# Kernel optimization log

Measured on AMD Instinct MI355X. Metric: run time of the kernel, lower is better.

## Reference

```python
import jax, jax.numpy as jnp
import numpy as np

FP8_MAX = 448.0  # float8_e4m3fn max normal
BLOCK = 128

def quant_dequant(x, block_size=BLOCK):
    """Block-wise fp8 (e4m3) activation/kernel quantization along last dim,
    immediately dequantized (mathematically equivalent to fp8 GEMM with
    per-block scales applied during accumulation)."""
    *lead, d = x.shape
    xb = x.reshape(*lead, d // block_size, block_size)
    scale = jnp.max(jnp.abs(xb), axis=-1, keepdims=True) / FP8_MAX
    scale = jnp.maximum(scale, 1e-12)
    q = (xb / scale).astype(jnp.float8_e4m3fn).astype(x.dtype)
    return (q * scale).reshape(x.shape)

def fp8_linear(x, W, b, block_size=BLOCK):
    y = jnp.dot(quant_dequant(x, block_size), quant_dequant(W, block_size))
    return y + b

def setup_inputs() -> dict:
    key = jax.random.key(0)
    ks = jax.random.split(key, 3)
    B, S, D = 2, 2048, 1024
    x = jax.random.normal(ks[0], (B, S, D), dtype=jnp.float32)
    W_qkv = jax.random.normal(ks[1], (D, 3 * D), dtype=jnp.float32) * (1.0 / np.sqrt(D))
    b_qkv = jnp.zeros((3 * D,), dtype=jnp.float32)
    W_out = jax.random.normal(ks[2], (D, D), dtype=jnp.float32) * (1.0 / np.sqrt(D))
    b_out = jnp.zeros((D,), dtype=jnp.float32)
    return {"x": x, "W_qkv": W_qkv, "b_qkv": b_qkv, "W_out": W_out, "b_out": b_out}

def reference(x, W_qkv, b_qkv, W_out, b_out):
    NUM_HEADS, HEAD_DIM = 16, 64
    B, S, _ = x.shape
    # fp8-quantized QKV projection
    qkv = fp8_linear(x, W_qkv, b_qkv)                       # [B,S,3*H*Dh]
    qkv = qkv.reshape(B, S, 3, NUM_HEADS, HEAD_DIM).transpose(2, 0, 3, 1, 4)
    q, k, v = qkv[0], qkv[1], qkv[2]                        # each [B,H,S,Dh]
    scale = 1.0 / jnp.sqrt(jnp.float32(HEAD_DIM)).astype(x.dtype)
    attn = jnp.einsum('bhqd,bhkd->bhqk', q, k) * scale      # [B,H,S,S]
    attn = jax.nn.softmax(attn, axis=-1)
    out = jnp.einsum('bhqk,bhkd->bhqd', attn, v)            # [B,H,S,Dh]
    out = out.transpose(0, 2, 1, 3).reshape(B, S, NUM_HEADS * HEAD_DIM)
    # fp8-quantized output projection; present (kv cache) is None here
    return fp8_linear(out, W_out, b_out)
```

## Files before the change

### kernel.cpp

```cpp
#include <hip/hip_runtime.h>
#include <cstdint>
#include <cstddef>

typedef __attribute__((ext_vector_type(8))) short bfrag;
typedef __attribute__((ext_vector_type(8))) _Float16 hfrag;
typedef __attribute__((ext_vector_type(2))) __fp16 fp16x2;
typedef __attribute__((ext_vector_type(4))) float f4;
typedef __attribute__((ext_vector_type(16))) float f16v;
typedef __attribute__((ext_vector_type(4))) unsigned short us4;

#define MFMA16H(a, b, c) __builtin_amdgcn_mfma_f32_16x16x32_f16(a, b, c, 0, 0, 0)
#define MFMA32H(a, b, c) __builtin_amdgcn_mfma_f32_32x32x16_f16(a, b, c, 0, 0, 0)

__device__ __forceinline__ unsigned cvt_pkrtz_u(float a, float b) {
  union { fp16x2 h; unsigned u; } c;
  c.h = __builtin_amdgcn_cvt_pkrtz(a, b);
  return c.u;
}
__device__ __forceinline__ unsigned short f2h_bits(float x) {
  _Float16 h = (_Float16)x;
  union { _Float16 h; unsigned short u; } c;
  c.h = h;
  return c.u;
}
__device__ __forceinline__ float h2f(unsigned short u) {
  union { unsigned short u; _Float16 h; } c;
  c.u = u;
  return (float)c.h;
}
__device__ __forceinline__ void permswap(unsigned& a, unsigned& b) {
  auto r = __builtin_amdgcn_permlane32_swap((int)a, (int)b, false, false);
  a = (unsigned)r[0];
  b = (unsigned)r[1];
}
__device__ __forceinline__ void gl16(const unsigned short* g, unsigned short* l) {
  __builtin_amdgcn_global_load_lds(
      (const __attribute__((address_space(1))) unsigned int*)g,
      (__attribute__((address_space(3))) unsigned int*)l, 16, 0, 0);
}
__device__ __forceinline__ float max3f(float a, float b, float c) {
  float r;
  asm("v_max3_f32 %0, %1, %2, %3" : "=v"(r) : "v"(a), "v"(b), "v"(c));
  return r;
}
__device__ __forceinline__ float exp2_fast(float x) {
  float r;
  asm("v_exp_f32 %0, %1" : "=v"(r) : "v"(x));
  return r;
}

__device__ __forceinline__ float qd_e4m3(float v) {
  float a = fabsf(v);
  unsigned u = __float_as_uint(a);
  int e = (int)(u >> 23) - 127;
  int k = e - 3;
  if (k < -9) k = -9;
  float big = __uint_as_float((unsigned)(k + 150) << 23);
  float r = (a + big) - big;
  return __builtin_copysignf(r, v);
}

__global__ __launch_bounds__(256) void quant_x(const float* __restrict__ src,
                                               unsigned short* __restrict__ q,
                                               float* __restrict__ s,
                                               int nblk) {
  int gid = blockIdx.x * 256 + threadIdx.x;
  int wid = gid >> 6;
  int lane = gid & 63;
  if (wid >= nblk) return;
  size_t off = (size_t)wid * 128 + lane * 2;
  float2 xv = *reinterpret_cast<const float2*>(src + off);
  float m = fmaxf(fabsf(xv.x), fabsf(xv.y));
#pragma unroll
  for (int d = 32; d > 0; d >>= 1) m = fmaxf(m, __shfl_xor(m, d));
  float scale = fmaxf(m / 448.0f, 1e-12f);
  unsigned short q0 = f2h_bits(qd_e4m3(xv.x / scale));
  unsigned short q1 = f2h_bits(qd_e4m3(xv.y / scale));
  *reinterpret_cast<unsigned*>(q + off) = (unsigned)q0 | ((unsigned)q1 << 16);
  if (lane == 0) s[wid] = scale;
}

__global__ __launch_bounds__(256) void quant_xh(const unsigned short* __restrict__ src,
                                                unsigned short* __restrict__ q,
                                                float* __restrict__ s,
                                                int nblk) {
  int gid = blockIdx.x * 256 + threadIdx.x;
  int wid = gid >> 6;
  int lane = gid & 63;
  if (wid >= nblk) return;
  size_t off = (size_t)wid * 128 + lane * 2;
  unsigned hv = *reinterpret_cast<const unsigned*>(src + off);
  float x0 = h2f((unsigned short)(hv & 0xffffu));
  float x1 = h2f((unsigned short)(hv >> 16));
  float m = fmaxf(fabsf(x0), fabsf(x1));
#pragma unroll
  for (int d = 32; d > 0; d >>= 1) m = fmaxf(m, __shfl_xor(m, d));
  float scale = fmaxf(m / 448.0f, 1e-12f);
  unsigned short q0 = f2h_bits(qd_e4m3(x0 / scale));
  unsigned short q1 = f2h_bits(qd_e4m3(x1 / scale));
  *reinterpret_cast<unsigned*>(q + off) = (unsigned)q0 | ((unsigned)q1 << 16);
  if (lane == 0) s[wid] = scale;
}

__global__ __launch_bounds__(256) void quant_w_t(const float* __restrict__ W,
                                                 unsigned short* __restrict__ WT,
                                                 int K, int N) {
  __shared__ __align__(16) unsigned short Ht[128][72];
  const int tid = threadIdx.x;
  const int w = tid >> 6, l = tid & 63;
  const int k0 = blockIdx.y * 64, n0 = blockIdx.x * 128;
#pragma unroll 4
  for (int i = 0; i < 16; ++i) {
    int kl = w * 16 + i;
    float2 xv = *reinterpret_cast<const float2*>(&W[(size_t)(k0 + kl) * N + n0 + l * 2]);
    float m = fmaxf(fabsf(xv.x), fabsf(xv.y));
#pragma unroll
    for (int d = 32; d > 0; d >>= 1) m = fmaxf(m, __shfl_xor(m, d));
    float scale = fmaxf(m / 448.0f, 1e-12f);
    Ht[l * 2][kl]     = f2h_bits(qd_e4m3(xv.x / scale) * scale);
    Ht[l * 2 + 1][kl] = f2h_bits(qd_e4m3(xv.y / scale) * scale);
  }
  __syncthreads();
  const int n = tid & 127, hs = tid >> 7;
  unsigned short* dst = WT + (size_t)(n0 + n) * K + k0 + hs * 32;
#pragma unroll
  for (int j = 0; j < 4; ++j)
    *reinterpret_cast<bfrag*>(dst + j * 8) =
        *reinterpret_cast<const bfrag*>(&Ht[n][hs * 32 + j * 8]);
}

template <int MF, bool SPLIT>
__global__ __launch_bounds__(256, 2) void gemm_q(const unsigned short* __restrict__ Aq,
                                                 const float* __restrict__ As,
                                                 const unsigned short* __restrict__ WT,
                                                 const float* __restrict__ bias,
                                                 float* __restrict__ Cf,
                                                 unsigned short* __restrict__ C16,
                                                 int M, int N, int K) {
  constexpr int MT = MF * 32;
  __shared__ __align__(16) unsigned short Al[MT][64];
  __shared__ __align__(16) unsigned short Bh[128][64];
  __shared__ float Ss[MT][8];
  const int tid = threadIdx.x;
  const int w = tid >> 6, l = tid & 63;
  const int lr = l & 15, lg = l >> 4;
  const int nbx = N >> 7;
  const int nwg = nbx * (M / MT);
  const int q8 = nwg >> 3;
  const int swz = ((int)blockIdx.x & 7) * q8 + ((int)blockIdx.x >> 3);
  const int row0 = (swz / nbx) * MT, col0 = (swz % nbx) << 7;
  const int wr = (w >> 1) * (MT / 2), wc = (w & 1) * 64;
  const int xsw = (lr & 7) * 8;

  if (MF == 4) {
    int r = tid >> 1, c0 = (tid & 1) * 4;
    *reinterpret_cast<float4*>(&Ss[r][c0]) =
        *reinterpret_cast<const float4*>(&As[(size_t)(row0 + r) * 8 + c0]);
  } else {
    int r = tid >> 2, c0 = (tid & 3) * 2;
    *reinterpret_cast<float2*>(&Ss[r][c0]) =
        *reinterpret_cast<const float2*>(&As[(size_t)(row0 + r) * 8 + c0]);
  }

  f4 acc[MF][4], seg[MF][4];
#pragma unroll
  for (int i = 0; i < MF; ++i)
#pragma unroll
    for (int j = 0; j < 4; ++j)
#pragma unroll
      for (int c = 0; c < 4; ++c) {
        acc[i][j][c] = 0.f;
        seg[i][j][c] = 0.f;
      }

  const int lrow = l >> 3;
  const int jch = (l & 7) ^ lrow;
  const unsigned short* pA = Aq + (size_t)(row0 + w * (MT / 4) + lrow) * K + jch * 8;
  const unsigned short* pH = WT + (size_t)(col0 + w * 32 + lrow) * K + jch * 8;
  unsigned short* dA = &Al[0][0] + w * (MT / 4) * 64;
  unsigned short* dH = &Bh[0][0] + w * 2048;

  const int niter = K >> 6;
  for (int it = 0; it < niter; ++it) {
    const int k0 = it << 6;
    __syncthreads();
#pragma unroll
    for (int ii = 0; ii < MF; ++ii)
      gl16(pA + (size_t)ii * 8 * K + k0, dA + ii * 512);
#pragma unroll
    for (int ii = 0; ii < 4; ++ii)
      gl16(pH + (size_t)ii * 8 * K + k0, dH + ii * 512);
    __syncthreads();

#pragma unroll
    for (int ks = 0; ks < 2; ++ks) {
      hfrag af[MF];
#pragma unroll
      for (int mf = 0; mf < MF; ++mf)
        af[mf] = *reinterpret_cast<const hfrag*>(
            &Al[0][0] + (wr + mf * 16 + lr) * 64 + ((ks * 32 + lg * 8) ^ xsw));
#pragma unroll
      for (int nf = 0; nf < 4; ++nf) {
        hfrag bh = *reinterpret_cast<const hfrag*>(
            &Bh[0][0] + (wc + nf * 16 + lr) * 64 + ((ks * 32 + lg * 8) ^ xsw));
#pragma unroll
        for (int mf = 0; mf < MF; ++mf)
          seg[mf][nf] = MFMA16H(af[mf], bh, seg[mf][nf]);
      }
    }

    if (it & 1) {
      const int kb = it >> 1;
#pragma unroll
      for (int mf = 0; mf < MF; ++mf) {
        float sv[4];
#pragma unroll
        for (int r = 0; r < 4; ++r) sv[r] = Ss[wr + mf * 16 + lg * 4 + r][kb];
#pragma unroll
        for (int nf = 0; nf < 4; ++nf)
#pragma unroll
          for (int r = 0; r < 4; ++r) {
            acc[mf][nf][r] += sv[r] * seg[mf][nf][r];
            seg[mf][nf][r] = 0.f;
          }
      }
    }
  }

#pragma unroll
  for (int mf = 0; mf < MF; ++mf) {
#pragma unroll
    for (int r = 0; r < 4; ++r) {
      const int m = row0 + wr + mf * 16 + lg * 4 + r;
#pragma unroll
      for (int nf = 0; nf < 4; ++nf) {
        const int col = col0 + wc + nf * 16 + lr;
        float o = acc[mf][nf][r] + bias[col];
        if (SPLIT) {
          C16[(size_t)m * N + col] = f2h_bits(o);
        } else {
          Cf[(size_t)m * N + col] = o;
        }
      }
    }
  }
}

__global__ __launch_bounds__(256, 2) void attn_mfma32(const unsigned short* __restrict__ qkv,
                                                      unsigned short* __restrict__ out16) {
  __shared__ __align__(16) unsigned short Vth[2][64][40];
  const int tid = threadIdx.x;
  const int w = tid >> 6, l = tid & 63;
  const int q = l & 31;
  const int hi = l >> 5;
  const int lin = (int)blockIdx.x;
  const int xcd = lin & 7, j = lin >> 3;
  const int bh = 4 * xcd + (j >> 4);
  const int qt = j & 15;
  const int q0 = qt * 128 + w * 32;
  const int b = bh >> 4, h = bh & 15;
  const size_t bbase = (size_t)b * 2048;
  const size_t hoff = (size_t)h * 64;
  const float C = 0.18033688011112042f;

  const int rA = (q & 24) | ((q + (q >> 3)) & 7);
  const int rB = 32 + ((q & 24) | ((q + 4 + (q >> 3)) & 7));

  hfrag qh[4];
  {
    const size_t qrow = (bbase + q0 + q) * 3072 + hoff + hi * 8;
#pragma unroll
    for (int f = 0; f < 4; ++f)
      qh[f] = *reinterpret_cast<const hfrag*>(qkv + qrow + f * 16);
  }

  const int skp = tid >> 3;
  const int sc = tid & 7;

  const unsigned short* kph = qkv + (bbase + q) * 3072 + 1024 + hoff + hi * 8;
  const unsigned short* vph = qkv + (bbase + skp) * 3072 + 2048 + hoff + sc * 8;
  const size_t KSTEP = (size_t)32 * 3072;

  hfrag kh[4];
  bfrag svh;

#pragma unroll
  for (int f = 0; f < 4; ++f)
    kh[f] = *reinterpret_cast<const hfrag*>(kph + f * 16);
  svh = *reinterpret_cast<const bfrag*>(vph);
  vph += KSTEP;
#pragma unroll
  for (int j2 = 0; j2 < 8; ++j2) {
    int row = sc * 8 + ((j2 + sc) & 7);
    Vth[0][row][skp] = (unsigned short)svh[j2];
  }
  f16v sA, sB;
#pragma unroll
  for (int r = 0; r < 16; ++r) sA[r] = 0.f;
  __builtin_amdgcn_s_setprio(1);
#pragma unroll
  for (int f = 0; f < 4; ++f) sA = MFMA32H(kh[f], qh[f], sA);
  __builtin_amdgcn_s_setprio(0);
  kph += KSTEP;
#pragma unroll
  for (int f = 0; f < 4; ++f)
    kh[f] = *reinterpret_cast<const hfrag*>(kph + f * 16);
  __syncthreads();

  f16v oA0, oA1;
#pragma unroll
  for (int r = 0; r < 16; ++r) { oA0[r] = 0.f; oA1[r] = 0.f; }
  float m2 = -1e30f, l_i = 0.f;

#define ATTN_ITER(KT, SCUR, SNXT)                                              \
  do {                                                                         \
    const int kt_ = (KT);                                                      \
    const int cur_ = kt_ & 1;                                                  \
         \
    if (kt_ < 63) {                                                            \
      _Pragma("unroll") for (int r = 0; r < 16; ++r) SNXT[r] = 0.f;            \
      __builtin_amdgcn_s_setprio(1);                                           \
      _Pragma("unroll") for (int f = 0; f < 4; ++f)                            \
          SNXT = MFMA32H(kh[f], qh[f], SNXT);                                  \
      __builtin_amdgcn_s_setprio(0);                                           \
    }                                                                          \
                                                         \
    if (kt_ < 62) {                                                            \
      kph += KSTEP;                                                            \
      _Pragma("unroll") for (int f = 0; f < 4; ++f)                            \
          kh[f] = *reinterpret_cast<const hfrag*>(kph + f * 16);               \
    }                                                                          \
                             \
    float t0 = max3f(SCUR[0], SCUR[1], SCUR[2]);                               \
    float t1 = max3f(SCUR[3], SCUR[4], SCUR[5]);                               \
    float t2 = max3f(SCUR[6], SCUR[7], SCUR[8]);                               \
    float t3 = max3f(SCUR[9], SCUR[10], SCUR[11]);                             \
    float t4 = max3f(SCUR[12], SCUR[13], SCUR[14]);                            \
    float u0 = max3f(t0, t1, SCUR[15]);                                        \
    float u1 = max3f(t2, t3, t4);                                              \
    float mt = fmaxf(u0, u1);                                                  \
    mt = fmaxf(mt, __shfl_xor(mt, 32));                                        \
    float mt2 = mt * C;                                                        \
    if (!__all(mt2 <= m2)) {           \
      float mn = fmaxf(m2, mt2);                                               \
      float corr = exp2_fast(m2 - mn);                                         \
      m2 = mn;                                                                 \
      l_i *= corr;                                                             \
      _Pragma("unroll") for (int r = 0; r < 16; ++r) {                         \
        oA0[r] *= corr; oA1[r] *= corr;                                        \
      }                                                                        \
    }                                                                          \
    float p[16];                                                               \
    _Pragma("unroll") for (int r = 0; r < 16; ++r)                             \
        p[r] = exp2_fast(fmaf(SCUR[r], C, -m2));                               \
    float r0_ = (p[0] + p[1]) + (p[2] + p[3]);                                 \
    float r1_ = (p[4] + p[5]) + (p[6] + p[7]);                                 \
    float r2_ = (p[8] + p[9]) + (p[10] + p[11]);                               \
    float r3_ = (p[12] + p[13]) + (p[14] + p[15]);                             \
    float rs = (r0_ + r1_) + (r2_ + r3_);                                      \
    rs += __shfl_xor(rs, 32);                                                  \
    l_i += rs;                                                                 \
                         \
    if (kt_ < 63) {                                                            \
      svh = *reinterpret_cast<const bfrag*>(vph);                              \
      vph += KSTEP;                                                            \
    }                                                                          \
                       \
    unsigned ph_[8];                                                           \
    _Pragma("unroll") for (int i = 0; i < 8; ++i)                              \
        ph_[i] = cvt_pkrtz_u(p[2 * i], p[2 * i + 1]);                          \
    permswap(ph_[0], ph_[2]); permswap(ph_[1], ph_[3]);                        \
    permswap(ph_[4], ph_[6]); permswap(ph_[5], ph_[7]);                        \
    union U4 { unsigned u[4]; hfrag f; };                                      \
    U4 f0h, f1h;                                                               \
    f0h.u[0] = ph_[0]; f0h.u[1] = ph_[1]; f0h.u[2] = ph_[2]; f0h.u[3] = ph_[3];\
    f1h.u[0] = ph_[4]; f1h.u[1] = ph_[5]; f1h.u[2] = ph_[6]; f1h.u[3] = ph_[7];\
                         \
    __builtin_amdgcn_s_setprio(1);                                             \
    _Pragma("unroll") for (int c = 0; c < 2; ++c) {                            \
      hfrag pF = c ? f1h.f : f0h.f;                                            \
      hfrag vh0 = *reinterpret_cast<const hfrag*>(&Vth[cur_][rA][c * 16 + hi * 8]); \
      hfrag vh1 = *reinterpret_cast<const hfrag*>(&Vth[cur_][rB][c * 16 + hi * 8]); \
      oA0 = MFMA32H(vh0, pF, oA0);                                             \
      oA1 = MFMA32H(vh1, pF, oA1);                                             \
    }                                                                          \
    __builtin_amdgcn_s_setprio(0);                                             \
              \
    if (kt_ < 63) {                                                            \
      _Pragma("unroll") for (int j2 = 0; j2 < 8; ++j2) {                       \
        int row = sc * 8 + ((j2 + sc) & 7);                                    \
        Vth[cur_ ^ 1][row][skp] = (unsigned short)svh[j2];                     \
      }                                                                        \
      __syncthreads();                                                         \
    }                                                                          \
  } while (0)

  for (int kt = 0; kt < 64; kt += 2) {
    ATTN_ITER(kt, sA, sB);
    ATTN_ITER(kt + 1, sB, sA);
  }
#undef ATTN_ITER

  float inv = 1.0f / l_i;
  const size_t orow = (bbase + q0 + q) * 1024 + hoff;
#pragma unroll
  for (int dblk = 0; dblk < 2; ++dblk) {
#pragma unroll
    for (int rg = 0; rg < 4; ++rg) {
      us4 o;
#pragma unroll
      for (int e = 0; e < 4; ++e) {
        float v = (dblk == 0 ? oA0[rg * 4 + e] : oA1[rg * 4 + e]) * inv;
        o[e] = f2h_bits(v);
      }
      *reinterpret_cast<us4*>(out16 + orow + dblk * 32 + rg * 8 + hi * 4) = o;
    }
  }
}

extern "C" void kernel_launch(void* const* d_in, const int* in_sizes, int n_in,
                              void* d_out, int out_size, void* d_ws, size_t ws_size,
                              hipStream_t stream) {
  const float* x     = (const float*)d_in[0];
  const float* W_qkv = (const float*)d_in[1];
  const float* b_qkv = (const float*)d_in[2];
  const float* W_out = (const float*)d_in[3];
  const float* b_out = (const float*)d_in[4];
  float* y = (float*)d_out;

  char* ws = (char*)d_ws;
  const size_t MB = 1u << 20;
  unsigned short* x_q   = (unsigned short*)(ws);
  float*          s_x   = (float*)(ws + 8 * MB);
  unsigned short* wqh   = (unsigned short*)(ws + 8 * MB + 256 * 1024);
  unsigned short* woh   = (unsigned short*)(ws + 20 * MB + 256 * 1024);
  unsigned short* qkv   = (unsigned short*)(ws + 24 * MB + 256 * 1024);
  unsigned short* y16   = (unsigned short*)(ws + 48 * MB + 256 * 1024);

  quant_x<<<8192, 256, 0, stream>>>(x, x_q, s_x, 32768);
  quant_w_t<<<dim3(24, 16), 256, 0, stream>>>(W_qkv, wqh, 1024, 3072);
  quant_w_t<<<dim3(8, 16), 256, 0, stream>>>(W_out, woh, 1024, 1024);

  gemm_q<4, true><<<768, 256, 0, stream>>>(x_q, s_x, wqh, b_qkv,
                                           nullptr, qkv, 4096, 3072, 1024);

  attn_mfma32<<<512, 256, 0, stream>>>(qkv, y16);

  quant_xh<<<8192, 256, 0, stream>>>(y16, x_q, s_x, 32768);

  gemm_q<2, false><<<512, 256, 0, stream>>>(x_q, s_x, woh, b_out,
                                            y, nullptr, 4096, 1024, 1024);
}
```

Before: 169.0 us.

## Double attention key tile to 64 keys per iteration

Processes 64 keys per iteration instead of 32. It computes two 32-key score blocks, does one shared max/rescale step, and stages two V sub-tiles into a widened shared buffer. This halves the number of __syncthreads, online-softmax correction checks and shuffle reductions across the key loop. In exchange it raises register pressure from the doubled K fragments, scores and probabilities, which at 2 blocks per SIMD-bound launch could cause spills or lower occupancy. The LDS padding changes from 40 to 68 columns, which may alter bank conflicts.

```diff
diff --git a/kernel.cpp b/kernel.cpp
--- a/kernel.cpp
+++ b/kernel.cpp
@@ -248,7 +248,7 @@
 
 __global__ __launch_bounds__(256, 2) void attn_mfma32(const unsigned short* __restrict__ qkv,
                                                       unsigned short* __restrict__ out16) {
-  __shared__ __align__(16) unsigned short Vth[2][64][40];
+  __shared__ __align__(16) unsigned short Vth[2][64][68];
   const int tid = threadIdx.x;
   const int w = tid >> 6, l = tid & 63;
   const int q = l & 31;
@@ -277,34 +277,48 @@
   const int skp = tid >> 3;
   const int sc = tid & 7;
 
+  const size_t SUB = (size_t)32 * 3072;
+  const size_t KSTEP = (size_t)64 * 3072;
   const unsigned short* kph = qkv + (bbase + q) * 3072 + 1024 + hoff + hi * 8;
   const unsigned short* vph = qkv + (bbase + skp) * 3072 + 2048 + hoff + sc * 8;
-  const size_t KSTEP = (size_t)32 * 3072;
-
-  hfrag kh[4];
-  bfrag svh;
-
-#pragma unroll
-  for (int f = 0; f < 4; ++f)
-    kh[f] = *reinterpret_cast<const hfrag*>(kph + f * 16);
-  svh = *reinterpret_cast<const bfrag*>(vph);
+
+  hfrag kh0[4], kh1[4];
+  bfrag svh0, svh1;
+
+#define VSTAGE(BUF)                                                            \
+  do {                                                                         \
+    _Pragma("unroll") for (int j2 = 0; j2 < 8; ++j2) {                         \
+      int row = sc * 8 + ((j2 + sc) & 7);                                      \
+      Vth[BUF][row][skp] = (unsigned short)svh0[j2];                           \
+      Vth[BUF][row][32 + skp] = (unsigned short)svh1[j2];                      \
+    }                                                                          \
+  } while (0)
+
+#pragma unroll
+  for (int f = 0; f < 4; ++f) {
+    kh0[f] = *reinterpret_cast<const hfrag*>(kph + f * 16);
+    kh1[f] = *reinterpret_cast<const hfrag*>(kph + SUB + f * 16);
+  }
+  svh0 = *reinterpret_cast<const bfrag*>(vph);
+  svh1 = *reinterpret_cast<const bfrag*>(vph + SUB);
   vph += KSTEP;
-#pragma unroll
-  for (int j2 = 0; j2 < 8; ++j2) {
-    int row = sc * 8 + ((j2 + sc) & 7);
-    Vth[0][row][skp] = (unsigned short)svh[j2];
-  }
-  f16v sA, sB;
-#pragma unroll
-  for (int r = 0; r < 16; ++r) sA[r] = 0.f;
+  VSTAGE(0);
+  f16v sA0, sA1, sB0, sB1;
+#pragma unroll
+  for (int r = 0; r < 16; ++r) { sA0[r] = 0.f; sA1[r] = 0.f; }
   __builtin_amdgcn_s_setprio(1);
 #pragma unroll
-  for (int f = 0; f < 4; ++f) sA = MFMA32H(kh[f], qh[f], sA);
+  for (int f = 0; f < 4; ++f) {
+    sA0 = MFMA32H(kh0[f], qh[f], sA0);
+    sA1 = MFMA32H(kh1[f], qh[f], sA1);
+  }
   __builtin_amdgcn_s_setprio(0);
   kph += KSTEP;
 #pragma unroll
-  for (int f = 0; f < 4; ++f)
-    kh[f] = *reinterpret_cast<const hfrag*>(kph + f * 16);
+  for (int f = 0; f < 4; ++f) {
+    kh0[f] = *reinterpret_cast<const hfrag*>(kph + f * 16);
+    kh1[f] = *reinterpret_cast<const hfrag*>(kph + SUB + f * 16);
+  }
   __syncthreads();
 
   f16v oA0, oA1;
@@ -312,33 +326,44 @@
   for (int r = 0; r < 16; ++r) { oA0[r] = 0.f; oA1[r] = 0.f; }
   float m2 = -1e30f, l_i = 0.f;
 
-#define ATTN_ITER(KT, SCUR, SNXT)                                              \
+#define ATTN_ITER(KT, SC0, SC1, SN0, SN1)                                      \
   do {                                                                         \
     const int kt_ = (KT);                                                      \
     const int cur_ = kt_ & 1;                                                  \
-         \
-    if (kt_ < 63) {                                                            \
-      _Pragma("unroll") for (int r = 0; r < 16; ++r) SNXT[r] = 0.f;            \
+                  \
+    if (kt_ < 31) {                                                            \
+      _Pragma("unroll") for (int r = 0; r < 16; ++r) { SN0[r] = 0.f; SN1[r] = 0.f; } \
       __builtin_amdgcn_s_setprio(1);                                           \
-      _Pragma("unroll") for (int f = 0; f < 4; ++f)                            \
-          SNXT = MFMA32H(kh[f], qh[f], SNXT);                                  \
+      _Pragma("unroll") for (int f = 0; f < 4; ++f) {                          \
+        SN0 = MFMA32H(kh0[f], qh[f], SN0);                                     \
+        SN1 = MFMA32H(kh1[f], qh[f], SN1);                                     \
+      }                                                                        \
       __builtin_amdgcn_s_setprio(0);                                           \
     }                                                                          \
                                                          \
-    if (kt_ < 62) {                                                            \
+    if (kt_ < 30) {                                                            \
       kph += KSTEP;                                                            \
-      _Pragma("unroll") for (int f = 0; f < 4; ++f)                            \
-          kh[f] = *reinterpret_cast<const hfrag*>(kph + f * 16);               \
-    }                                                                          \
-                             \
-    float t0 = max3f(SCUR[0], SCUR[1], SCUR[2]);                               \
-    float t1 = max3f(SCUR[3], SCUR[4], SCUR[5]);                               \
-    float t2 = max3f(SCUR[6], SCUR[7], SCUR[8]);                               \
-    float t3 = max3f(SCUR[9], SCUR[10], SCUR[11]);                             \
-    float t4 = max3f(SCUR[12], SCUR[13], SCUR[14]);                            \
-    float u0 = max3f(t0, t1, SCUR[15]);                                        \
+      _Pragma("unroll") for (int f = 0; f < 4; ++f) {                          \
+        kh0[f] = *reinterpret_cast<const hfrag*>(kph + f * 16);                \
+        kh1[f] = *reinterpret_cast<const hfrag*>(kph + SUB + f * 16);          \
+      }                                                                        \
+    }                                                                          \
+                \
+    float t0 = max3f(SC0[0], SC0[1], SC0[2]);                                  \
+    float t1 = max3f(SC0[3], SC0[4], SC0[5]);                                  \
+    float t2 = max3f(SC0[6], SC0[7], SC0[8]);                                  \
+    float t3 = max3f(SC0[9], SC0[10], SC0[11]);                                \
+    float t4 = max3f(SC0[12], SC0[13], SC0[14]);                               \
+    float t5 = max3f(SC1[0], SC1[1], SC1[2]);                                  \
+    float t6 = max3f(SC1[3], SC1[4], SC1[5]);                                  \
+    float t7 = max3f(SC1[6], SC1[7], SC1[8]);                                  \
+    float t8 = max3f(SC1[9], SC1[10], SC1[11]);                                \
+    float t9 = max3f(SC1[12], SC1[13], SC1[14]);                               \
+    float u0 = max3f(t0, t1, SC0[15]);                                         \
     float u1 = max3f(t2, t3, t4);                                              \
-    float mt = fmaxf(u0, u1);                                                  \
+    float u2 = max3f(t5, t6, SC1[15]);                                         \
+    float u3 = max3f(t7, t8, t9);                                              \
+    float mt = fmaxf(max3f(u0, u1, u2), u3);                                   \
     mt = fmaxf(mt, __shfl_xor(mt, 32));                                        \
     float mt2 = mt * C;                                                        \
     if (!__all(mt2 <= m2)) {           \
@@ -350,56 +375,72 @@
         oA0[r] *= corr; oA1[r] *= corr;                                        \
       }                                                                        \
     }                                                                          \
-    float p[16];                                                               \
-    _Pragma("unroll") for (int r = 0; r < 16; ++r)                             \
-        p[r] = exp2_fast(fmaf(SCUR[r], C, -m2));                               \
-    float r0_ = (p[0] + p[1]) + (p[2] + p[3]);                                 \
-    float r1_ = (p[4] + p[5]) + (p[6] + p[7]);                                 \
-    float r2_ = (p[8] + p[9]) + (p[10] + p[11]);                               \
-    float r3_ = (p[12] + p[13]) + (p[14] + p[15]);                             \
-    float rs = (r0_ + r1_) + (r2_ + r3_);                                      \
+    float p0[16], p1[16];                                                      \
+    _Pragma("unroll") for (int r = 0; r < 16; ++r) {                           \
+      p0[r] = exp2_fast(fmaf(SC0[r], C, -m2));                                 \
+      p1[r] = exp2_fast(fmaf(SC1[r], C, -m2));                                 \
+    }                                                                          \
+    float ra_ = ((p0[0] + p0[1]) + (p0[2] + p0[3])) +                          \
+                ((p0[4] + p0[5]) + (p0[6] + p0[7]));                           \
+    float rb_ = ((p0[8] + p0[9]) + (p0[10] + p0[11])) +                        \
+                ((p0[12] + p0[13]) + (p0[14] + p0[15]));                       \
+    float rc_ = ((p1[0] + p1[1]) + (p1[2] + p1[3])) +                          \
+                ((p1[4] + p1[5]) + (p1[6] + p1[7]));                           \
+    float rd_ = ((p1[8] + p1[9]) + (p1[10] + p1[11])) +                        \
+                ((p1[12] + p1[13]) + (p1[14] + p1[15]));                       \
+    float rs = (ra_ + rb_) + (rc_ + rd_);                                      \
     rs += __shfl_xor(rs, 32);                                                  \
     l_i += rs;                                                                 \
-                         \
-    if (kt_ < 63) {                                                            \
-      svh = *reinterpret_cast<const bfrag*>(vph);                              \
+                        \
+    if (kt_ < 31) {                                                            \
+      svh0 = *reinterpret_cast<const bfrag*>(vph);                             \
+      svh1 = *reinterpret_cast<const bfrag*>(vph + SUB);                       \
       vph += KSTEP;                                                            \
     }                                                                          \
+       \
+    unsigned pa_[8], pb_[8];                                                   \
+    _Pragma("unroll") for (int i = 0; i < 8; ++i) {                            \
+      pa_[i] = cvt_pkrtz_u(p0[2 * i], p0[2 * i + 1]);                          \
+      pb_[i] = cvt_pkrtz_u(p1[2 * i], p1[2 * i + 1]);                          \
+    }                                                                          \
+    permswap(pa_[0], pa_[2]); permswap(pa_[1], pa_[3]);                        \
+    permswap(pa_[4], pa_[6]); permswap(pa_[5], pa_[7]);                        \
+    permswap(pb_[0], pb_[2]); permswap(pb_[1], pb_[3]);                        \
+    permswap(pb_[4], pb_[6]); permswap(pb_[5], pb_[7]);                        \
+    union U4 { unsigned u[4]; hfrag f; };                                      \
+    U4 f0h, f1h, f2h, f3h;                                                     \
+    f0h.u[0] = pa_[0]; f0h.u[1] = pa_[1]; f0h.u[2] = pa_[2]; f0h.u[3] = pa_[3];\
+    f1h.u[0] = pa_[4]; f1h.u[1] = pa_[5]; f1h.u[2] = pa_[6]; f1h.u[3] = pa_[7];\
+    f2h.u[0] = pb_[0]; f2h.u[1] = pb_[1]; f2h.u[2] = pb_[2]; f2h.u[3] = pb_[3];\
+    f3h.u[0] = pb_[4]; f3h.u[1] = pb_[5]; f3h.u[2] = pb_[6]; f3h.u[3] = pb_[7];\
                        \
-    unsigned ph_[8];                                                           \
-    _Pragma("unroll") for (int i = 0; i < 8; ++i)                              \
-        ph_[i] = cvt_pkrtz_u(p[2 * i], p[2 * i + 1]);                          \
-    permswap(ph_[0], ph_[2]); permswap(ph_[1], ph_[3]);                        \
-    permswap(ph_[4], ph_[6]); permswap(ph_[5], ph_[7]);                        \
-    union U4 { unsigned u[4]; hfrag f; };                                      \
-    U4 f0h, f1h;                                                               \
-    f0h.u[0] = ph_[0]; f0h.u[1] = ph_[1]; f0h.u[2] = ph_[2]; f0h.u[3] = ph_[3];\
-    f1h.u[0] = ph_[4]; f1h.u[1] = ph_[5]; f1h.u[2] = ph_[6]; f1h.u[3] = ph_[7];\
-                         \
     __builtin_amdgcn_s_setprio(1);                                             \
     _Pragma("unroll") for (int c = 0; c < 2; ++c) {                            \
-      hfrag pF = c ? f1h.f : f0h.f;                                            \
-      hfrag vh0 = *reinterpret_cast<const hfrag*>(&Vth[cur_][rA][c * 16 + hi * 8]); \
-      hfrag vh1 = *reinterpret_cast<const hfrag*>(&Vth[cur_][rB][c * 16 + hi * 8]); \
-      oA0 = MFMA32H(vh0, pF, oA0);                                             \
-      oA1 = MFMA32H(vh1, pF, oA1);                                             \
+      hfrag pF0 = c ? f1h.f : f0h.f;                                           \
+      hfrag pF1 = c ? f3h.f : f2h.f;                                           \
+      hfrag vA0 = *reinterpret_cast<const hfrag*>(&Vth[cur_][rA][c * 16 + hi * 8]);      \
+      hfrag vA1 = *reinterpret_cast<const hfrag*>(&Vth[cur_][rA][32 + c * 16 + hi * 8]); \
+      hfrag vB0 = *reinterpret_cast<const hfrag*>(&Vth[cur_][rB][c * 16 + hi * 8]);      \
+      hfrag vB1 = *reinterpret_cast<const hfrag*>(&Vth[cur_][rB][32 + c * 16 + hi * 8]); \
+      oA0 = MFMA32H(vA0, pF0, oA0);                                            \
+      oA1 = MFMA32H(vB0, pF0, oA1);                                            \
+      oA0 = MFMA32H(vA1, pF1, oA0);                                            \
+      oA1 = MFMA32H(vB1, pF1, oA1);                                            \
     }                                                                          \
     __builtin_amdgcn_s_setprio(0);                                             \
               \
-    if (kt_ < 63) {                                                            \
-      _Pragma("unroll") for (int j2 = 0; j2 < 8; ++j2) {                       \
-        int row = sc * 8 + ((j2 + sc) & 7);                                    \
-        Vth[cur_ ^ 1][row][skp] = (unsigned short)svh[j2];                     \
-      }                                                                        \
+    if (kt_ < 31) {                                                            \
+      VSTAGE(cur_ ^ 1);                                                        \
       __syncthreads();                                                         \
     }                                                                          \
   } while (0)
 
-  for (int kt = 0; kt < 64; kt += 2) {
-    ATTN_ITER(kt, sA, sB);
-    ATTN_ITER(kt + 1, sB, sA);
+  for (int kt = 0; kt < 32; kt += 2) {
+    ATTN_ITER(kt, sA0, sA1, sB0, sB1);
+    ATTN_ITER(kt + 1, sB0, sB1, sA0, sA1);
   }
 #undef ATTN_ITER
+#undef VSTAGE
 
   float inv = 1.0f / l_i;
   const size_t orow = (bbase + q0 + q) * 1024 + hoff;
```

Result: slower. 172.8 us (+2.3%).
